# Performance work log

Measured on AMD Instinct MI355X. Metric: run time of the kernel, lower is better.

The kernel has to match this reference:

```python
import jax, jax.numpy as jnp
import numpy as np

D_MODEL = 1024
NUM_HEADS = 16
D_K = D_MODEL // NUM_HEADS


def setup_inputs() -> dict:
    key = jax.random.key(0)
    ks = jax.random.split(key, 5)
    x = jax.random.normal(ks[0], (8, 1024, D_MODEL), dtype=jnp.float32)
    s_in = 1.0 / np.sqrt(D_MODEL)
    W_qkv = jax.random.normal(ks[1], (D_MODEL, 3 * D_MODEL), dtype=jnp.float32) * s_in
    b_qkv = jax.random.normal(ks[2], (3 * D_MODEL,), dtype=jnp.float32) * 0.01
    W_o = jax.random.normal(ks[3], (D_MODEL, D_MODEL), dtype=jnp.float32) * s_in
    b_o = jax.random.normal(ks[4], (D_MODEL,), dtype=jnp.float32) * 0.01
    return {"x": x, "W_qkv": W_qkv, "b_qkv": b_qkv, "W_o": W_o, "b_o": b_o}


def reference(x, W_qkv, b_qkv, W_o, b_o):
    B, N, D = x.shape
    qkv = x @ W_qkv + b_qkv                      # [B, N, 3D]
    qkv = qkv.reshape(B, N, 3, NUM_HEADS, D_K)
    qkv = jnp.transpose(qkv, (2, 0, 3, 1, 4))    # [3, B, H, N, d_k]
    q, k, v = qkv[0], qkv[1], qkv[2]
    scale = 1.0 / np.sqrt(D_K).astype(np.float32)
    attn = jnp.einsum('bhqd,bhkd->bhqk', q, k) * scale
    attn = jax.nn.softmax(attn, axis=-1)
    out = jnp.einsum('bhqk,bhkd->bhqd', attn, v)  # [B, H, N, d_k]
    out = jnp.transpose(out, (0, 2, 1, 3)).reshape(B, N, D)
    return out @ W_o + b_o
```

## Files before the change

kernel.cpp:

```cpp
#include <hip/hip_runtime.h>


typedef __attribute__((ext_vector_type(8))) short bf16x8;
typedef __attribute__((ext_vector_type(4))) float f32x4;

#define GLOAD_LDS16(gp, lp)                                                              \
  __builtin_amdgcn_global_load_lds((const __attribute__((address_space(1))) void*)(gp),  \
                                   (__attribute__((address_space(3))) void*)(lp), 16, 0, 0)

__device__ __forceinline__ unsigned short f2bf(float f) {
  unsigned int u = __float_as_uint(f);
  u += 0x7fffu + ((u >> 16) & 1u);
  return (unsigned short)(u >> 16);
}

__global__ __launch_bounds__(256) void prep_fused(
    const float* __restrict__ x, unsigned short* __restrict__ x_bf,
    const float* __restrict__ W_qkv, unsigned short* __restrict__ wqkv_t,
    const float* __restrict__ W_o, unsigned short* __restrict__ wo_t) {
  const int b = blockIdx.x;
  if (b < 2048) {
    const int n4 = 8388608 / 4;
    for (int i = b * 256 + threadIdx.x; i < n4; i += 2048 * 256) {
      float4 v = reinterpret_cast<const float4*>(x)[i];
      ushort4 o;
      o.x = f2bf(v.x); o.y = f2bf(v.y); o.z = f2bf(v.z); o.w = f2bf(v.w);
      reinterpret_cast<ushort4*>(x_bf)[i] = o;
    }
  } else {
    __shared__ float tile[32][33];
    const float* W;
    unsigned short* Wt;
    int R = 1024, C, bx, by;
    if (b < 5120) {
      W = W_qkv; Wt = wqkv_t; C = 3072;
      int bb = b - 2048; bx = bb % 96; by = bb / 96;
    } else {
      W = W_o; Wt = wo_t; C = 1024;
      int bb = b - 5120; bx = bb & 31; by = bb >> 5;
    }
    const int tx = threadIdx.x & 31, ty = threadIdx.x >> 5;
    const int c0 = bx * 32, r0 = by * 32;
    #pragma unroll
    for (int i = 0; i < 4; i++) {
      int r = r0 + ty + i * 8;
      tile[ty + i * 8][tx] = W[(size_t)r * C + c0 + tx];
    }
    __syncthreads();
    #pragma unroll
    for (int i = 0; i < 4; i++) {
      int c = c0 + ty + i * 8;
      Wt[(size_t)c * R + r0 + tx] = f2bf(tile[tx][ty + i * 8]);
    }
  }
}

template <int MODE>
__global__ __launch_bounds__(512) void gemm256(
    const unsigned short* __restrict__ A, const unsigned short* __restrict__ Bt,
    const float* __restrict__ bias, unsigned short* __restrict__ qkv_out,
    float* __restrict__ Cout) {
  __shared__ __align__(16) unsigned short As[3][128 * 64];
  __shared__ __align__(16) unsigned short Bs[3][256 * 64];
  const int t = threadIdx.x;
  const int lane = t & 63, wid = t >> 6;
  const int lr = lane & 15, g = lane >> 4;
  const int wm = wid >> 2, wn = wid & 3;

  const int nwg = gridDim.x * gridDim.y;
  const int id = blockIdx.x + gridDim.x * blockIdx.y;
  const int sw = (id & 7) * (nwg >> 3) + (id >> 3);
  const int bx = sw % gridDim.x, by = sw / gridDim.x;
  const int row0 = by * 128, col0 = bx * 256;

  const int srow = t >> 3, sch = t & 7;

  auto stA = [&](int buf, int kt, int j) {
    int row = j * 64 + srow;
    int ch = sch ^ (row & 7);
    GLOAD_LDS16(A + (size_t)(row0 + row) * 1024 + kt * 64 + ch * 8,
                (char*)&As[buf][0] + j * 8192 + t * 16);
  };
  auto stB = [&](int buf, int kt, int j) {
    int row = j * 64 + srow;
    int ch = sch ^ (row & 7);
    GLOAD_LDS16(Bt + (size_t)(col0 + row) * 1024 + kt * 64 + ch * 8,
                (char*)&Bs[buf][0] + j * 8192 + t * 16);
  };
  auto rdA = [&](int buf, int c, int m) -> bf16x8 {
    int r = wm * 64 + m * 16 + lr;
    return *(const bf16x8*)((const char*)&As[buf][0] + r * 128 +
                            ((c * 64 + g * 16) ^ ((r & 7) << 4)));
  };
  auto rdB = [&](int buf, int c, int n) -> bf16x8 {
    int r = wn * 64 + n * 16 + lr;
    return *(const bf16x8*)((const char*)&Bs[buf][0] + r * 128 +
                            ((c * 64 + g * 16) ^ ((r & 7) << 4)));
  };

  f32x4 acc[4][4] = {};

  stA(0, 0, 0); stA(0, 0, 1);
  stB(0, 0, 0); stB(0, 0, 1); stB(0, 0, 2); stB(0, 0, 3);
  stA(1, 1, 0); stA(1, 1, 1);
  stB(1, 1, 0); stB(1, 1, 1); stB(1, 1, 2); stB(1, 1, 3);
  asm volatile("s_waitcnt vmcnt(6)" ::: "memory");
  __builtin_amdgcn_s_barrier();

  for (int kt = 0; kt < 16; kt++) {
    const int buf = kt % 3;
    const int bufn = (kt + 2) % 3;
    const bool pf = (kt <= 13);
    if (kt > 0) {
      if (kt == 15) asm volatile("s_waitcnt vmcnt(0)" ::: "memory");
      else          asm volatile("s_waitcnt vmcnt(6)" ::: "memory");
      __builtin_amdgcn_s_barrier();
    }

    bf16x8 a0[4], b0[4];
    #pragma unroll
    for (int m = 0; m < 4; m++) a0[m] = rdA(buf, 0, m);
    #pragma unroll
    for (int n = 0; n < 4; n++) b0[n] = rdB(buf, 0, n);
    if (pf) { stA(bufn, kt + 2, 0); stA(bufn, kt + 2, 1); stB(bufn, kt + 2, 0); }
    __builtin_amdgcn_s_barrier();
    asm volatile("s_waitcnt lgkmcnt(0)" ::: "memory");
    __builtin_amdgcn_sched_barrier(0);
    __builtin_amdgcn_s_setprio(1);
    #pragma unroll
    for (int m = 0; m < 4; m++)
      #pragma unroll
      for (int n = 0; n < 4; n++)
        acc[m][n] = __builtin_amdgcn_mfma_f32_16x16x32_bf16(a0[m], b0[n], acc[m][n], 0, 0, 0);
    __builtin_amdgcn_s_setprio(0);
    __builtin_amdgcn_s_barrier();

    bf16x8 a1[4], b1[4];
    #pragma unroll
    for (int m = 0; m < 4; m++) a1[m] = rdA(buf, 1, m);
    #pragma unroll
    for (int n = 0; n < 4; n++) b1[n] = rdB(buf, 1, n);
    if (pf) { stB(bufn, kt + 2, 1); stB(bufn, kt + 2, 2); stB(bufn, kt + 2, 3); }
    __builtin_amdgcn_s_barrier();
    asm volatile("s_waitcnt lgkmcnt(0)" ::: "memory");
    __builtin_amdgcn_sched_barrier(0);
    __builtin_amdgcn_s_setprio(1);
    #pragma unroll
    for (int m = 0; m < 4; m++)
      #pragma unroll
      for (int n = 0; n < 4; n++)
        acc[m][n] = __builtin_amdgcn_mfma_f32_16x16x32_bf16(a1[m], b1[n], acc[m][n], 0, 0, 0);
    __builtin_amdgcn_s_setprio(0);
    __builtin_amdgcn_s_barrier();
  }

  if (MODE == 0) {
    const int which = col0 >> 10;
    if (which == 2) {
      #pragma unroll
      for (int m = 0; m < 4; m++) {
        int row = row0 + wm * 64 + m * 16 + g * 4;
        int bb = row >> 10, nn = row & 1023;
        #pragma unroll
        for (int n = 0; n < 4; n++) {
          int col = col0 + wn * 64 + n * 16 + lr;
          int cc = col & 1023;
          int h = cc >> 6, dk = cc & 63;
          float bv = bias[col];
          ushort4 w;
          w.x = f2bf(acc[m][n][0] + bv);
          w.y = f2bf(acc[m][n][1] + bv);
          w.z = f2bf(acc[m][n][2] + bv);
          w.w = f2bf(acc[m][n][3] + bv);
          size_t idx = ((size_t)2 << 23) + (((size_t)(bb * 16 + h)) << 16) +
                       (size_t)dk * 1024 + nn;
          *(ushort4*)(qkv_out + idx) = w;
        }
      }
    } else {
      #pragma unroll
      for (int m = 0; m < 4; m++) {
        #pragma unroll
        for (int n = 0; n < 4; n++) {
          int col = col0 + wn * 64 + n * 16 + lr;
          int cc = col & 1023;
          int h = cc >> 6, dk = cc & 63;
          #pragma unroll
          for (int r = 0; r < 4; r++) {
            int row = row0 + wm * 64 + m * 16 + g * 4 + r;
            int bb = row >> 10, nn = row & 1023;
            float v = acc[m][n][r] + bias[col];
            if (which == 0) v *= 0.125f;
            size_t idx = ((size_t)which << 23) +
                         (((size_t)((bb * 16 + h) * 1024 + nn)) << 6) + dk;
            qkv_out[idx] = f2bf(v);
          }
        }
      }
    }
  } else {
    #pragma unroll
    for (int m = 0; m < 4; m++) {
      #pragma unroll
      for (int n = 0; n < 4; n++) {
        int col = col0 + wn * 64 + n * 16 + lr;
        #pragma unroll
        for (int r = 0; r < 4; r++) {
          int row = row0 + wm * 64 + m * 16 + g * 4 + r;
          Cout[(size_t)row * 1024 + col] = acc[m][n][r] + bias[col];
        }
      }
    }
  }
}

__global__ __launch_bounds__(512) void attn_mfma(
    const unsigned short* __restrict__ qkv, unsigned short* __restrict__ attn_out) {
  __shared__ __align__(16) unsigned short K_lds[2][64 * 64];
  __shared__ __align__(16) unsigned short V_lds[2][64 * 64];
  __shared__ __align__(16) unsigned short P_lds[128 * 64];

  const int bid = ((blockIdx.x & 7) << 7) + (blockIdx.x >> 3);
  const int bh = bid >> 3, qt = bid & 7;
  const unsigned short* Qp = qkv + ((size_t)bh << 16);
  const unsigned short* Kp = qkv + (1u << 23) + ((size_t)bh << 16);
  const unsigned short* Vt = qkv + (2u << 23) + ((size_t)bh << 16);

  const int t = threadIdx.x;
  const int lane = t & 63, wid = t >> 6;
  const int lr = lane & 15, g = lane >> 4;

  bf16x8 qf[2];
  {
    int qrow = qt * 128 + wid * 16 + lr;
    qf[0] = *(const bf16x8*)(Qp + (size_t)qrow * 64 + g * 8);
    qf[1] = *(const bf16x8*)(Qp + (size_t)qrow * 64 + 32 + g * 8);
  }

  const int srow = t >> 3;
  const int sch  = (t & 7) ^ (srow & 7);
  const int so   = t * 16;

  auto stage = [&](int buf, int kt) {
    GLOAD_LDS16(Kp + (size_t)(kt * 64 + srow) * 64 + sch * 8, (char*)&K_lds[buf][0] + so);
    GLOAD_LDS16(Vt + (size_t)srow * 1024 + kt * 64 + sch * 8, (char*)&V_lds[buf][0] + so);
  };

  f32x4 o_acc[4] = {};
  float den[4] = {0.f, 0.f, 0.f, 0.f};

  stage(0, 0);
  __syncthreads();
  int buf = 0;
  for (int kt = 0; kt < 16; kt++) {
    if (kt + 1 < 16) stage(buf ^ 1, kt + 1);

    f32x4 s4[4] = {};
    __builtin_amdgcn_s_setprio(1);
    #pragma unroll
    for (int ks = 0; ks < 4; ks++) {
      int krow = ks * 16 + lr;
      #pragma unroll
      for (int c = 0; c < 2; c++) {
        bf16x8 kf = *(const bf16x8*)((char*)&K_lds[buf][0] + krow * 128 +
                                     ((c * 64 + g * 16) ^ ((krow & 7) << 4)));
        s4[ks] = __builtin_amdgcn_mfma_f32_16x16x32_bf16(qf[c], kf, s4[ks], 0, 0, 0);
      }
    }
    __builtin_amdgcn_s_setprio(0);

    #pragma unroll
    for (int ks = 0; ks < 4; ks++) {
      #pragma unroll
      for (int r = 0; r < 4; r++) {
        float e = __expf(s4[ks][r]);
        den[r] += e;
        int q = wid * 16 + g * 4 + r;
        *(unsigned short*)((char*)P_lds + q * 128 +
                           (((ks * 16 + lr) * 2) ^ ((q & 7) << 4))) = f2bf(e);
      }
    }

    bf16x8 pa[2];
    {
      int q = wid * 16 + lr;
      #pragma unroll
      for (int c = 0; c < 2; c++)
        pa[c] = *(const bf16x8*)((char*)P_lds + q * 128 +
                                 ((c * 64 + g * 16) ^ ((q & 7) << 4)));
    }
    __builtin_amdgcn_s_setprio(1);
    #pragma unroll
    for (int ds_ = 0; ds_ < 4; ds_++) {
      int drow = ds_ * 16 + lr;
      #pragma unroll
      for (int c = 0; c < 2; c++) {
        bf16x8 vf = *(const bf16x8*)((char*)&V_lds[buf][0] + drow * 128 +
                                     ((c * 64 + g * 16) ^ ((drow & 7) << 4)));
        o_acc[ds_] = __builtin_amdgcn_mfma_f32_16x16x32_bf16(pa[c], vf, o_acc[ds_], 0, 0, 0);
      }
    }
    __builtin_amdgcn_s_setprio(0);
    __syncthreads();
    buf ^= 1;
  }

  #pragma unroll
  for (int r = 0; r < 4; r++) {
    den[r] += __shfl_xor(den[r], 1, 64);
    den[r] += __shfl_xor(den[r], 2, 64);
    den[r] += __shfl_xor(den[r], 4, 64);
    den[r] += __shfl_xor(den[r], 8, 64);
  }

  const int bb = bh >> 4, h = bh & 15;
  #pragma unroll
  for (int ds_ = 0; ds_ < 4; ds_++) {
    #pragma unroll
    for (int r = 0; r < 4; r++) {
      int q = qt * 128 + wid * 16 + g * 4 + r;
      int d = h * 64 + ds_ * 16 + lr;
      attn_out[((size_t)(bb * 1024 + q)) * 1024 + d] = f2bf(o_acc[ds_][r] / den[r]);
    }
  }
}

extern "C" void kernel_launch(void* const* d_in, const int* in_sizes, int n_in,
                              void* d_out, int out_size, void* d_ws, size_t ws_size,
                              hipStream_t stream) {
  const float* x     = (const float*)d_in[0];
  const float* W_qkv = (const float*)d_in[1];
  const float* b_qkv = (const float*)d_in[2];
  const float* W_o   = (const float*)d_in[3];
  const float* b_o   = (const float*)d_in[4];
  float* out = (float*)d_out;

  unsigned short* ws      = (unsigned short*)d_ws;
  unsigned short* x_bf    = ws;
  unsigned short* wqkv_t  = x_bf + 8388608;
  unsigned short* wo_t    = wqkv_t + 3145728;
  unsigned short* qkv     = wo_t + 1048576;
  unsigned short* attn_o  = qkv + 25165824;

  prep_fused<<<6144, 256, 0, stream>>>(x, x_bf, W_qkv, wqkv_t, W_o, wo_t);
  gemm256<0><<<dim3(12, 64), 512, 0, stream>>>(x_bf, wqkv_t, b_qkv, qkv, nullptr);
  attn_mfma<<<1024, 512, 0, stream>>>(qkv, attn_o);
  gemm256<1><<<dim3(4, 64), 512, 0, stream>>>(attn_o, wo_t, b_o, nullptr, out);
}
```

Baseline: 157.8 us.

## Double attention query tile to 256 rows per block for K/V reuse

Each attention block now handles 256 query rows instead of 128, with every wave computing two 16-row MFMA sub-tiles that share the same K and V fragments loaded from LDS. The grid drops from 1024 to 512 blocks and the block-id swizzle and P buffer are resized to match. This halves global K/V staging traffic and LDS fragment reads per output. In exchange it doubles accumulator registers per thread, enlarges LDS use, and gives the 256-CU device only two blocks per CU, which may reduce occupancy and latency hiding.

```diff
diff --git a/kernel.cpp b/kernel.cpp
--- a/kernel.cpp
+++ b/kernel.cpp
@@ -218,10 +218,10 @@
     const unsigned short* __restrict__ qkv, unsigned short* __restrict__ attn_out) {
   __shared__ __align__(16) unsigned short K_lds[2][64 * 64];
   __shared__ __align__(16) unsigned short V_lds[2][64 * 64];
-  __shared__ __align__(16) unsigned short P_lds[128 * 64];
-
-  const int bid = ((blockIdx.x & 7) << 7) + (blockIdx.x >> 3);
-  const int bh = bid >> 3, qt = bid & 7;
+  __shared__ __align__(16) unsigned short P_lds[256 * 64];
+
+  const int bid = ((blockIdx.x & 7) << 6) + (blockIdx.x >> 3);
+  const int bh = bid >> 2, qt = bid & 3;
   const unsigned short* Qp = qkv + ((size_t)bh << 16);
   const unsigned short* Kp = qkv + (1u << 23) + ((size_t)bh << 16);
   const unsigned short* Vt = qkv + (2u << 23) + ((size_t)bh << 16);
@@ -230,11 +230,12 @@
   const int lane = t & 63, wid = t >> 6;
   const int lr = lane & 15, g = lane >> 4;
 
-  bf16x8 qf[2];
-  {
-    int qrow = qt * 128 + wid * 16 + lr;
-    qf[0] = *(const bf16x8*)(Qp + (size_t)qrow * 64 + g * 8);
-    qf[1] = *(const bf16x8*)(Qp + (size_t)qrow * 64 + 32 + g * 8);
+  bf16x8 qf[2][2];
+  #pragma unroll
+  for (int m = 0; m < 2; m++) {
+    int qrow = qt * 256 + wid * 32 + m * 16 + lr;
+    qf[m][0] = *(const bf16x8*)(Qp + (size_t)qrow * 64 + g * 8);
+    qf[m][1] = *(const bf16x8*)(Qp + (size_t)qrow * 64 + 32 + g * 8);
   }
 
   const int srow = t >> 3;
@@ -246,8 +247,8 @@
     GLOAD_LDS16(Vt + (size_t)srow * 1024 + kt * 64 + sch * 8, (char*)&V_lds[buf][0] + so);
   };
 
-  f32x4 o_acc[4] = {};
-  float den[4] = {0.f, 0.f, 0.f, 0.f};
+  f32x4 o_acc[2][4] = {};
+  float den[2][4] = {};
 
   stage(0, 0);
   __syncthreads();
@@ -255,7 +256,7 @@
   for (int kt = 0; kt < 16; kt++) {
     if (kt + 1 < 16) stage(buf ^ 1, kt + 1);
 
-    f32x4 s4[4] = {};
+    f32x4 s4[2][4] = {};
     __builtin_amdgcn_s_setprio(1);
     #pragma unroll
     for (int ks = 0; ks < 4; ks++) {
@@ -264,30 +265,36 @@
       for (int c = 0; c < 2; c++) {
         bf16x8 kf = *(const bf16x8*)((char*)&K_lds[buf][0] + krow * 128 +
                                      ((c * 64 + g * 16) ^ ((krow & 7) << 4)));
-        s4[ks] = __builtin_amdgcn_mfma_f32_16x16x32_bf16(qf[c], kf, s4[ks], 0, 0, 0);
+        #pragma unroll
+        for (int m = 0; m < 2; m++)
+          s4[m][ks] = __builtin_amdgcn_mfma_f32_16x16x32_bf16(qf[m][c], kf, s4[m][ks], 0, 0, 0);
       }
     }
     __builtin_amdgcn_s_setprio(0);
 
     #pragma unroll
-    for (int ks = 0; ks < 4; ks++) {
-      #pragma unroll
-      for (int r = 0; r < 4; r++) {
-        float e = __expf(s4[ks][r]);
-        den[r] += e;
-        int q = wid * 16 + g * 4 + r;
-        *(unsigned short*)((char*)P_lds + q * 128 +
-                           (((ks * 16 + lr) * 2) ^ ((q & 7) << 4))) = f2bf(e);
-      }
-    }
-
-    bf16x8 pa[2];
-    {
-      int q = wid * 16 + lr;
+    for (int m = 0; m < 2; m++) {
+      #pragma unroll
+      for (int ks = 0; ks < 4; ks++) {
+        #pragma unroll
+        for (int r = 0; r < 4; r++) {
+          float e = __expf(s4[m][ks][r]);
+          den[m][r] += e;
+          int q = wid * 32 + m * 16 + g * 4 + r;
+          *(unsigned short*)((char*)P_lds + q * 128 +
+                             (((ks * 16 + lr) * 2) ^ ((q & 7) << 4))) = f2bf(e);
+        }
+      }
+    }
+
+    bf16x8 pa[2][2];
+    #pragma unroll
+    for (int m = 0; m < 2; m++) {
+      int q = wid * 32 + m * 16 + lr;
       #pragma unroll
       for (int c = 0; c < 2; c++)
-        pa[c] = *(const bf16x8*)((char*)P_lds + q * 128 +
-                                 ((c * 64 + g * 16) ^ ((q & 7) << 4)));
+        pa[m][c] = *(const bf16x8*)((char*)P_lds + q * 128 +
+                                    ((c * 64 + g * 16) ^ ((q & 7) << 4)));
     }
     __builtin_amdgcn_s_setprio(1);
     #pragma unroll
@@ -297,7 +304,9 @@
       for (int c = 0; c < 2; c++) {
         bf16x8 vf = *(const bf16x8*)((char*)&V_lds[buf][0] + drow * 128 +
                                      ((c * 64 + g * 16) ^ ((drow & 7) << 4)));
-        o_acc[ds_] = __builtin_amdgcn_mfma_f32_16x16x32_bf16(pa[c], vf, o_acc[ds_], 0, 0, 0);
+        #pragma unroll
+        for (int m = 0; m < 2; m++)
+          o_acc[m][ds_] = __builtin_amdgcn_mfma_f32_16x16x32_bf16(pa[m][c], vf, o_acc[m][ds_], 0, 0, 0);
       }
     }
     __builtin_amdgcn_s_setprio(0);
@@ -306,21 +315,26 @@
   }
 
   #pragma unroll
-  for (int r = 0; r < 4; r++) {
-    den[r] += __shfl_xor(den[r], 1, 64);
-    den[r] += __shfl_xor(den[r], 2, 64);
-    den[r] += __shfl_xor(den[r], 4, 64);
-    den[r] += __shfl_xor(den[r], 8, 64);
-  }
+  for (int m = 0; m < 2; m++)
+    #pragma unroll
+    for (int r = 0; r < 4; r++) {
+      den[m][r] += __shfl_xor(den[m][r], 1, 64);
+      den[m][r] += __shfl_xor(den[m][r], 2, 64);
+      den[m][r] += __shfl_xor(den[m][r], 4, 64);
+      den[m][r] += __shfl_xor(den[m][r], 8, 64);
+    }
 
   const int bb = bh >> 4, h = bh & 15;
   #pragma unroll
-  for (int ds_ = 0; ds_ < 4; ds_++) {
-    #pragma unroll
-    for (int r = 0; r < 4; r++) {
-      int q = qt * 128 + wid * 16 + g * 4 + r;
-      int d = h * 64 + ds_ * 16 + lr;
-      attn_out[((size_t)(bb * 1024 + q)) * 1024 + d] = f2bf(o_acc[ds_][r] / den[r]);
+  for (int m = 0; m < 2; m++) {
+    #pragma unroll
+    for (int ds_ = 0; ds_ < 4; ds_++) {
+      #pragma unroll
+      for (int r = 0; r < 4; r++) {
+        int q = qt * 256 + wid * 32 + m * 16 + g * 4 + r;
+        int d = h * 64 + ds_ * 16 + lr;
+        attn_out[((size_t)(bb * 1024 + q)) * 1024 + d] = f2bf(o_acc[m][ds_][r] / den[m][r]);
+      }
     }
   }
 }
@@ -344,6 +358,6 @@
 
   prep_fused<<<6144, 256, 0, stream>>>(x, x_bf, W_qkv, wqkv_t, W_o, wo_t);
   gemm256<0><<<dim3(12, 64), 512, 0, stream>>>(x_bf, wqkv_t, b_qkv, qkv, nullptr);
-  attn_mfma<<<1024, 512, 0, stream>>>(qkv, attn_o);
+  attn_mfma<<<512, 512, 0, stream>>>(qkv, attn_o);
   gemm256<1><<<dim3(4, 64), 512, 0, stream>>>(attn_o, wo_t, b_o, nullptr, out);
 }
```

New measurement: 164.5 us. +4.2%, slower.
